# Kernel tuning notes

Hardware: AMD Instinct MI355X
Metric: run time of the kernel (lower is better)

The kernel has to match this reference:

```python
import jax, jax.numpy as jnp
import numpy as np

N, FIN, F, H = 4096, 128, 64, 8
NEG = -1e10


def setup_inputs() -> dict:
    key = jax.random.key(0)
    ks = jax.random.split(key, 6)
    X = jax.random.normal(ks[0], (N, FIN), dtype=jnp.float32)
    # sparse-ish binary adjacency with self loops, stored dense (as the layer expects)
    A = (jax.random.uniform(ks[1], (N, N)) < 0.05).astype(jnp.int32)
    A = A.at[jnp.arange(N), jnp.arange(N)].set(1)
    W = jax.random.normal(ks[2], (H, FIN, F), dtype=jnp.float32) * (1.0 / np.sqrt(FIN))
    b = jnp.zeros((H, F), dtype=jnp.float32)
    a_self = jax.random.normal(ks[3], (H, F), dtype=jnp.float32) * (1.0 / np.sqrt(F))
    a_neigh = jax.random.normal(ks[4], (H, F), dtype=jnp.float32) * (1.0 / np.sqrt(F))
    return {"X": X, "A": A, "W": W, "b": b, "a_self": a_self, "a_neigh": a_neigh}


def reference(X, A, W, b, a_self, a_neigh):
    # Dropout layers run in inference mode in the original call -> identity.
    feats = jnp.einsum('nf,hfo->hno', X, W)              # [H, N, F]
    s_self = jnp.einsum('hno,ho->hn', feats, a_self)     # [H, N]
    s_neigh = jnp.einsum('hno,ho->hn', feats, a_neigh)   # [H, N]
    scores = s_self[:, :, None] + s_neigh[:, None, :]    # [H, N, N]
    scores = jnp.where(scores > 0, scores, 0.2 * scores)  # LeakyReLU(0.2)
    mask = (1.0 - A.astype(jnp.float32)) * NEG            # [N, N]
    attn = jax.nn.softmax(scores + mask[None], axis=-1)   # [H, N, N]
    out = jnp.einsum('hnm,hmo->hno', attn, feats) + b[:, None, :]
    out = jax.nn.elu(out)                                 # [H, N, F]
    # concat heads -> [N, H*F]
    return jnp.transpose(out, (1, 0, 2)).reshape(N, H * F)
```

## Files before the change

### kernel.cpp

```cpp
#include <hip/hip_runtime.h>
#include <cmath>


#define NN 4096
#define FIN 128
#define FF 64
#define HH 8

typedef _Float16 h2 __attribute__((ext_vector_type(2)));
typedef _Float16 h4 __attribute__((ext_vector_type(4)));
typedef _Float16 h8 __attribute__((ext_vector_type(8)));
typedef float f32x2 __attribute__((ext_vector_type(2)));
typedef float f32x4 __attribute__((ext_vector_type(4)));

union H8 {
  h8 v;
  h2 p[4];
};
union H4 {
  h4 v;
  h2 p[2];
};

__global__ __launch_bounds__(256) void pack_kernel(
    const int* __restrict__ A, const float* __restrict__ W,
    const float* __restrict__ X, unsigned long long* __restrict__ bitsT,
    _Float16* __restrict__ Wsw, _Float16* __restrict__ Xsw) {
  const int b = blockIdx.x;
  const int tid = threadIdx.x;
  const int wave = tid >> 6, lane = tid & 63;
  if (b < NN) {
    __shared__ int ldsT[4][4][256];
    const int* ar = A + (size_t)b * NN;
    int4 v[4];
#pragma unroll
    for (int it = 0; it < 4; ++it) {
      const int g = wave * 4 + it;
      v[it] = *(const int4*)(ar + g * 256 + lane * 4);
    }
#pragma unroll
    for (int it = 0; it < 4; ++it) *(int4*)&ldsT[wave][it][lane * 4] = v[it];
#pragma unroll
    for (int it = 0; it < 4; ++it) {
      const int g = wave * 4 + it;
      int w0 = ldsT[wave][it][0 * 64 + lane];
      int w1 = ldsT[wave][it][1 * 64 + lane];
      int w2 = ldsT[wave][it][2 * 64 + lane];
      int w3 = ldsT[wave][it][3 * 64 + lane];
      unsigned long long m0 = __ballot(w0 != 0);
      unsigned long long m1 = __ballot(w1 != 0);
      unsigned long long m2 = __ballot(w2 != 0);
      unsigned long long m3 = __ballot(w3 != 0);
      if (lane == 0) {
        bitsT[(size_t)(g * 4 + 0) * NN + b] = m0;
        bitsT[(size_t)(g * 4 + 1) * NN + b] = m1;
        bitsT[(size_t)(g * 4 + 2) * NN + b] = m2;
        bitsT[(size_t)(g * 4 + 3) * NN + b] = m3;
      }
    }
  } else if (b < NN + 2) {
    const int h0 = (b - NN) * 4;
    for (int h = h0; h < h0 + 4; ++h) {
      for (int c = tid; c < 1024; c += 256) {
        int ln = c & 63, nb = (c >> 6) & 3, kt = c >> 8;
        int f = nb * 16 + (ln & 15);
        int k0 = kt * 32 + (ln >> 4) * 8;
        h8 v;
#pragma unroll
        for (int j = 0; j < 8; ++j)
          v[j] = (_Float16)W[((size_t)(h * FIN) + k0 + j) * FF + f];
        *(h8*)(Wsw + ((size_t)(((h * 4 + kt) * 4 + nb) * 64 + ln)) * 8) = v;
      }
    }
  } else {
    const int tile = (b - NN - 2) * 4 + wave;
    const int l16 = lane & 15, quad = lane >> 4;
    const float* xr = X + (size_t)(tile * 16 + l16) * FIN;
#pragma unroll
    for (int kt = 0; kt < 4; ++kt) {
      int k0 = kt * 32 + quad * 8;
      f32x4 x0 = *(const f32x4*)(xr + k0);
      f32x4 x1 = *(const f32x4*)(xr + k0 + 4);
      h8 v = {(_Float16)x0[0], (_Float16)x0[1], (_Float16)x0[2],
              (_Float16)x0[3], (_Float16)x1[0], (_Float16)x1[1],
              (_Float16)x1[2], (_Float16)x1[3]};
      *(h8*)(Xsw + ((size_t)((tile * 4 + kt) * 64 + lane)) * 8) = v;
    }
  }
}

__global__ __launch_bounds__(256) void feats_kernel(
    const _Float16* __restrict__ Xsw, const _Float16* __restrict__ Wsw,
    const float* __restrict__ a_self, const float* __restrict__ a_neigh,
    _Float16* __restrict__ feats_sw, _Float16* __restrict__ es_h,
    _Float16* __restrict__ esn_h, _Float16* __restrict__ et_h,
    _Float16* __restrict__ etn_h) {
  const int h = blockIdx.y;
  const int tid = threadIdx.x, wave = tid >> 6, lane = tid & 63;
  const int l16 = lane & 15, quad = lane >> 4;
  const int rt = blockIdx.x * 4 + wave;
  const int r0 = rt * 16;

  f32x4 acc[4];
#pragma unroll
  for (int nb = 0; nb < 4; ++nb) acc[nb] = (f32x4){0.f, 0.f, 0.f, 0.f};

  const _Float16* xp = Xsw + ((size_t)(rt * 4) * 64 + lane) * 8;
  const _Float16* wp = Wsw + ((size_t)(h * 16) * 64 + lane) * 8;
  h8 Af[4];
#pragma unroll
  for (int kt = 0; kt < 4; ++kt) Af[kt] = *(const h8*)(xp + kt * 512);
#pragma unroll
  for (int kt = 0; kt < 4; ++kt)
#pragma unroll
    for (int nb = 0; nb < 4; ++nb) {
      h8 Bf = *(const h8*)(wp + (kt * 4 + nb) * 512);
      acc[nb] = __builtin_amdgcn_mfma_f32_16x16x32_f16(Af[kt], Bf, acc[nb], 0, 0, 0);
    }

  float as[4], an[4];
#pragma unroll
  for (int nb = 0; nb < 4; ++nb) {
    as[nb] = a_self[h * FF + nb * 16 + l16];
    an[nb] = a_neigh[h * FF + nb * 16 + l16];
  }
#pragma unroll
  for (int r = 0; r < 4; ++r) {
    float ps = acc[0][r] * as[0] + acc[1][r] * as[1] + acc[2][r] * as[2] +
               acc[3][r] * as[3];
    float pn = acc[0][r] * an[0] + acc[1][r] * an[1] + acc[2][r] * an[2] +
               acc[3][r] * an[3];
#pragma unroll
    for (int m = 1; m <= 8; m <<= 1) {
      ps += __shfl_xor(ps, m, 64);
      pn += __shfl_xor(pn, m, 64);
    }
    if (l16 == 0) {
      int node = h * NN + r0 + quad * 4 + r;
      es_h[node] = (_Float16)__expf(ps - 2.0f);
      esn_h[node] = (_Float16)__expf(0.2f * ps - 2.0f);
      et_h[node] = (_Float16)__expf(pn - 2.0f);
      etn_h[node] = (_Float16)__expf(0.2f * pn - 2.0f);
    }
  }

  const int kb = r0 >> 5;
  const int quadA = ((r0 >> 4) & 1) * 2 + (quad >> 1);
  const int jbase = (quad & 1) << 2;
#pragma unroll
  for (int nb = 0; nb < 4; ++nb) {
    h4 v = {(_Float16)acc[nb][0], (_Float16)acc[nb][1], (_Float16)acc[nb][2],
            (_Float16)acc[nb][3]};
    size_t off = ((size_t)((h * 128 + kb) * 4 + nb) << 9) +
                 ((quadA * 16 + l16) << 3) + jbase;
    *(h4*)(feats_sw + off) = v;
  }
}

__global__ __launch_bounds__(256, 2) void attn_kernel(
    const unsigned long long* __restrict__ bitsT,
    const _Float16* __restrict__ feats_sw, const _Float16* __restrict__ es_h,
    const _Float16* __restrict__ esn_h, const _Float16* __restrict__ et_h,
    const _Float16* __restrict__ etn_h, const float* __restrict__ bias,
    float* __restrict__ out) {
  const int bid = blockIdx.x;
  const int h = bid & 7, n0 = (bid >> 3) << 6;
  const int tid = threadIdx.x, wave = tid >> 6, lane = tid & 63;
  const int l16 = lane & 15, quad = lane >> 4;

  __shared__ h4 lut16[16];
  __shared__ float accL[4][16][66];
  __shared__ float denL[4][64];
  if (tid < 16) {
    h4 m;
#pragma unroll
    for (int j = 0; j < 4; ++j) m[j] = (_Float16)((tid >> j) & 1);
    lut16[tid] = m;
  }
  __syncthreads();

  h2 esp[4], esnp[4];
#pragma unroll
  for (int rg = 0; rg < 4; ++rg) {
    _Float16 e = es_h[h * NN + n0 + rg * 16 + l16];
    _Float16 en = esn_h[h * NN + n0 + rg * 16 + l16];
    esp[rg] = (h2){e, e};
    esnp[rg] = (h2){en, en};
  }

  f32x4 acc[4][4];
  f32x4 accd[4];
#pragma unroll
  for (int rg = 0; rg < 4; ++rg) {
    accd[rg] = (f32x4){0.f, 0.f, 0.f, 0.f};
#pragma unroll
    for (int nb = 0; nb < 4; ++nb) acc[rg][nb] = (f32x4){0.f, 0.f, 0.f, 0.f};
  }
  const h8 onesB = {(_Float16)1.f, (_Float16)1.f, (_Float16)1.f,
                    (_Float16)1.f, (_Float16)1.f, (_Float16)1.f,
                    (_Float16)1.f, (_Float16)1.f};

  const unsigned long long* btb = bitsT + n0 + l16;
  const _Float16* etp = et_h + h * NN + (quad << 3);
  const _Float16* etnp = etn_h + h * NN + (quad << 3);
  const _Float16* fb = feats_sw + ((size_t)h << 18) + (lane << 3);

#pragma unroll 2
  for (int ct = wave; ct < 64; ct += 4) {
    uint2 bits[4];
#pragma unroll
    for (int rg = 0; rg < 4; ++rg)
      bits[rg] = *(const uint2*)(btb + (size_t)ct * NN + rg * 16);
    const _Float16* fbt = fb + ((size_t)ct << 12);
#pragma unroll
    for (int kf = 0; kf < 2; ++kf) {
      H8 ET, ETN;
      ET.v = *(const h8*)(etp + (ct << 6) + kf * 32);
      ETN.v = *(const h8*)(etnp + (ct << 6) + kf * 32);
      const _Float16* fk = fbt + (kf << 11);
      h8 B0 = *(const h8*)(fk);
      h8 B1 = *(const h8*)(fk + 512);
      h8 B2 = *(const h8*)(fk + 1024);
      h8 B3 = *(const h8*)(fk + 1536);
#pragma unroll
      for (int rg = 0; rg < 4; ++rg) {
        unsigned word = kf ? bits[rg].y : bits[rg].x;
        unsigned byt = (word >> (quad << 3)) & 0xFFu;
        H4 mlo, mhi;
        mlo.v = lut16[byt & 15u];
        mhi.v = lut16[byt >> 4];
        H8 P;
#pragma unroll
        for (int p = 0; p < 4; ++p) {
          h2 a = esp[rg] * ET.p[p];
          h2 b = esnp[rg] * ETN.p[p];
          h2 r = __builtin_elementwise_max(a, b);
          P.p[p] = r * (p < 2 ? mlo.p[p] : mhi.p[p - 2]);
        }
        acc[rg][0] =
            __builtin_amdgcn_mfma_f32_16x16x32_f16(P.v, B0, acc[rg][0], 0, 0, 0);
        acc[rg][1] =
            __builtin_amdgcn_mfma_f32_16x16x32_f16(P.v, B1, acc[rg][1], 0, 0, 0);
        acc[rg][2] =
            __builtin_amdgcn_mfma_f32_16x16x32_f16(P.v, B2, acc[rg][2], 0, 0, 0);
        acc[rg][3] =
            __builtin_amdgcn_mfma_f32_16x16x32_f16(P.v, B3, acc[rg][3], 0, 0, 0);
        accd[rg] =
            __builtin_amdgcn_mfma_f32_16x16x32_f16(P.v, onesB, accd[rg], 0, 0, 0);
      }
    }
  }

  if (l16 == 0) {
#pragma unroll
    for (int rg = 0; rg < 4; ++rg)
#pragma unroll
      for (int r = 0; r < 4; ++r)
        denL[wave][rg * 16 + quad * 4 + r] = accd[rg][r];
  }

  const int erow = tid >> 4, ec0 = (tid & 15) << 2;
#pragma unroll
  for (int ph = 0; ph < 4; ++ph) {
    __syncthreads();
#pragma unroll
    for (int nb = 0; nb < 4; ++nb)
#pragma unroll
      for (int r = 0; r < 4; ++r)
        accL[wave][quad * 4 + r][nb * 16 + l16] = acc[ph][nb][r];
    __syncthreads();
    const int grow = ph * 16 + erow;
    float dn = denL[0][grow] + denL[1][grow] + denL[2][grow] + denL[3][grow];
    float inv = 1.0f / dn;
    f32x2 v0 = (f32x2){0.f, 0.f}, v1 = (f32x2){0.f, 0.f};
#pragma unroll
    for (int w = 0; w < 4; ++w) {
      v0 += *(const f32x2*)&accL[w][erow][ec0];
      v1 += *(const f32x2*)&accL[w][erow][ec0 + 2];
    }
    const f32x4 bv = *(const f32x4*)(bias + h * FF + ec0);
    f32x4 v = {v0[0], v0[1], v1[0], v1[1]};
#pragma unroll
    for (int i = 0; i < 4; ++i) {
      float x = v[i] * inv + bv[i];
      v[i] = x > 0.f ? x : (__expf(x) - 1.0f);
    }
    *(f32x4*)(out + (size_t)(n0 + grow) * (HH * FF) + h * FF + ec0) = v;
  }
}

extern "C" void kernel_launch(void* const* d_in, const int* in_sizes, int n_in,
                              void* d_out, int out_size, void* d_ws,
                              size_t ws_size, hipStream_t stream) {
  const float* X = (const float*)d_in[0];
  const int* A = (const int*)d_in[1];
  const float* W = (const float*)d_in[2];
  const float* b = (const float*)d_in[3];
  const float* a_self = (const float*)d_in[4];
  const float* a_neigh = (const float*)d_in[5];
  float* out = (float*)d_out;

  char* ws = (char*)d_ws;
  unsigned long long* bitsT = (unsigned long long*)ws;
  _Float16* feats_sw = (_Float16*)(ws + (2u << 20));
  _Float16* es_h = (_Float16*)(ws + (6u << 20));
  _Float16* esn_h = (_Float16*)(ws + (6u << 20) + (64u << 10));
  _Float16* et_h = (_Float16*)(ws + (6u << 20) + (128u << 10));
  _Float16* etn_h = (_Float16*)(ws + (6u << 20) + (192u << 10));
  _Float16* Wsw = (_Float16*)(ws + (6u << 20) + (256u << 10));
  _Float16* Xsw = (_Float16*)(ws + (6u << 20) + (384u << 10));

  pack_kernel<<<NN + 66, 256, 0, stream>>>(A, W, X, bitsT, Wsw, Xsw);
  feats_kernel<<<dim3(64, 8), 256, 0, stream>>>(Xsw, Wsw, a_self, a_neigh,
                                                feats_sw, es_h, esn_h, et_h,
                                                etn_h);
  attn_kernel<<<512, 256, 0, stream>>>(bitsT, feats_sw, es_h, esn_h, et_h,
                                       etn_h, b, out);
}
```

Measured before the change: 145.5 us.

## Software-pipeline feature and mask loads with register double buffering in attention loop

Replaces the unroll-2 column-tile loop with an explicit ping-pong scheme that holds two register sets of feature fragments and adjacency bits. The loads for the next tile are issued before the MFMA compute on the current one, so global memory latency can hide behind matrix work. This raises register pressure (16 h8 plus 8 uint2 live values) under launch_bounds(256,2), which could cause spills or lower occupancy.

```diff
diff --git a/kernel.cpp b/kernel.cpp
--- a/kernel.cpp
+++ b/kernel.cpp
@@ -157,6 +157,65 @@
   }
 }
 
+
+#define LOADSET(p0, p1, p2, p3, p4, p5, p6, p7, q0, q1, q2, q3, CT)          \
+  {                                                                          \
+    const _Float16* fk_ = fb + ((size_t)(CT) << 12);                         \
+    p0 = *(const h8*)(fk_);                                                  \
+    p1 = *(const h8*)(fk_ + 512);                                            \
+    p2 = *(const h8*)(fk_ + 1024);                                           \
+    p3 = *(const h8*)(fk_ + 1536);                                           \
+    p4 = *(const h8*)(fk_ + 2048);                                           \
+    p5 = *(const h8*)(fk_ + 2560);                                           \
+    p6 = *(const h8*)(fk_ + 3072);                                           \
+    p7 = *(const h8*)(fk_ + 3584);                                           \
+    const unsigned long long* bp_ = btb + (size_t)(CT) * NN;                 \
+    q0 = *(const uint2*)(bp_);                                               \
+    q1 = *(const uint2*)(bp_ + 16);                                          \
+    q2 = *(const uint2*)(bp_ + 32);                                          \
+    q3 = *(const uint2*)(bp_ + 48);                                          \
+  }
+
+#define KFBODY(ET_, ETN_, B0_, B1_, B2_, B3_, w0_, w1_, w2_, w3_)            \
+  {                                                                          \
+    const unsigned ww_[4] = {w0_, w1_, w2_, w3_};                            \
+    _Pragma("unroll") for (int rg = 0; rg < 4; ++rg) {                       \
+      unsigned byt_ = (ww_[rg] >> (quad << 3)) & 0xFFu;                      \
+      H4 mlo_, mhi_;                                                         \
+      mlo_.v = lut16[byt_ & 15u];                                            \
+      mhi_.v = lut16[byt_ >> 4];                                             \
+      H8 P_;                                                                 \
+      _Pragma("unroll") for (int p = 0; p < 4; ++p) {                        \
+        h2 a_ = esp[rg] * ET_.p[p];                                          \
+        h2 b_ = esnp[rg] * ETN_.p[p];                                        \
+        h2 r_ = __builtin_elementwise_max(a_, b_);                           \
+        P_.p[p] = r_ * (p < 2 ? mlo_.p[p] : mhi_.p[p - 2]);                  \
+      }                                                                      \
+      acc[rg][0] =                                                           \
+          __builtin_amdgcn_mfma_f32_16x16x32_f16(P_.v, B0_, acc[rg][0], 0, 0, 0); \
+      acc[rg][1] =                                                           \
+          __builtin_amdgcn_mfma_f32_16x16x32_f16(P_.v, B1_, acc[rg][1], 0, 0, 0); \
+      acc[rg][2] =                                                           \
+          __builtin_amdgcn_mfma_f32_16x16x32_f16(P_.v, B2_, acc[rg][2], 0, 0, 0); \
+      acc[rg][3] =                                                           \
+          __builtin_amdgcn_mfma_f32_16x16x32_f16(P_.v, B3_, acc[rg][3], 0, 0, 0); \
+      accd[rg] =                                                             \
+          __builtin_amdgcn_mfma_f32_16x16x32_f16(P_.v, onesB, accd[rg], 0, 0, 0); \
+    }                                                                        \
+  }
+
+#define COMPUTE(p0, p1, p2, p3, p4, p5, p6, p7, q0, q1, q2, q3, CT)          \
+  {                                                                          \
+    const int ct_ = (CT);                                                    \
+    H8 ET0_, ETN0_, ET1_, ETN1_;                                             \
+    ET0_.v = *(const h8*)(etp + (ct_ << 6));                                 \
+    ETN0_.v = *(const h8*)(etnp + (ct_ << 6));                               \
+    ET1_.v = *(const h8*)(etp + (ct_ << 6) + 32);                            \
+    ETN1_.v = *(const h8*)(etnp + (ct_ << 6) + 32);                          \
+    KFBODY(ET0_, ETN0_, p0, p1, p2, p3, q0.x, q1.x, q2.x, q3.x)              \
+    KFBODY(ET1_, ETN1_, p4, p5, p6, p7, q0.y, q1.y, q2.y, q3.y)              \
+  }
+
 __global__ __launch_bounds__(256, 2) void attn_kernel(
     const unsigned long long* __restrict__ bitsT,
     const _Float16* __restrict__ feats_sw, const _Float16* __restrict__ es_h,
@@ -205,50 +264,23 @@
   const _Float16* etnp = etn_h + h * NN + (quad << 3);
   const _Float16* fb = feats_sw + ((size_t)h << 18) + (lane << 3);
 
-#pragma unroll 2
-  for (int ct = wave; ct < 64; ct += 4) {
-    uint2 bits[4];
-#pragma unroll
-    for (int rg = 0; rg < 4; ++rg)
-      bits[rg] = *(const uint2*)(btb + (size_t)ct * NN + rg * 16);
-    const _Float16* fbt = fb + ((size_t)ct << 12);
-#pragma unroll
-    for (int kf = 0; kf < 2; ++kf) {
-      H8 ET, ETN;
-      ET.v = *(const h8*)(etp + (ct << 6) + kf * 32);
-      ETN.v = *(const h8*)(etnp + (ct << 6) + kf * 32);
-      const _Float16* fk = fbt + (kf << 11);
-      h8 B0 = *(const h8*)(fk);
-      h8 B1 = *(const h8*)(fk + 512);
-      h8 B2 = *(const h8*)(fk + 1024);
-      h8 B3 = *(const h8*)(fk + 1536);
-#pragma unroll
-      for (int rg = 0; rg < 4; ++rg) {
-        unsigned word = kf ? bits[rg].y : bits[rg].x;
-        unsigned byt = (word >> (quad << 3)) & 0xFFu;
-        H4 mlo, mhi;
-        mlo.v = lut16[byt & 15u];
-        mhi.v = lut16[byt >> 4];
-        H8 P;
-#pragma unroll
-        for (int p = 0; p < 4; ++p) {
-          h2 a = esp[rg] * ET.p[p];
-          h2 b = esnp[rg] * ETN.p[p];
-          h2 r = __builtin_elementwise_max(a, b);
-          P.p[p] = r * (p < 2 ? mlo.p[p] : mhi.p[p - 2]);
-        }
-        acc[rg][0] =
-            __builtin_amdgcn_mfma_f32_16x16x32_f16(P.v, B0, acc[rg][0], 0, 0, 0);
-        acc[rg][1] =
-            __builtin_amdgcn_mfma_f32_16x16x32_f16(P.v, B1, acc[rg][1], 0, 0, 0);
-        acc[rg][2] =
-            __builtin_amdgcn_mfma_f32_16x16x32_f16(P.v, B2, acc[rg][2], 0, 0, 0);
-        acc[rg][3] =
-            __builtin_amdgcn_mfma_f32_16x16x32_f16(P.v, B3, acc[rg][3], 0, 0, 0);
-        accd[rg] =
-            __builtin_amdgcn_mfma_f32_16x16x32_f16(P.v, onesB, accd[rg], 0, 0, 0);
-      }
-    }
+  h8 xa0, xa1, xa2, xa3, xa4, xa5, xa6, xa7;
+  h8 xb0, xb1, xb2, xb3, xb4, xb5, xb6, xb7;
+  uint2 qa0, qa1, qa2, qa3, qb0, qb1, qb2, qb3;
+
+  LOADSET(xa0, xa1, xa2, xa3, xa4, xa5, xa6, xa7, qa0, qa1, qa2, qa3, wave)
+#pragma unroll 1
+  for (int i = 0; i < 8; ++i) {
+    const int cta = wave + i * 8;
+    LOADSET(xb0, xb1, xb2, xb3, xb4, xb5, xb6, xb7, qb0, qb1, qb2, qb3,
+            cta + 4)
+    COMPUTE(xa0, xa1, xa2, xa3, xa4, xa5, xa6, xa7, qa0, qa1, qa2, qa3, cta)
+    if (i < 7) {
+      LOADSET(xa0, xa1, xa2, xa3, xa4, xa5, xa6, xa7, qa0, qa1, qa2, qa3,
+              cta + 8)
+    }
+    COMPUTE(xb0, xb1, xb2, xb3, xb4, xb5, xb6, xb7, qb0, qb1, qb2, qb3,
+            cta + 4)
   }
 
   if (l16 == 0) {
```

Result: no change. 146.0 us (+0.4%).
